# Performance work log

Measured on AMD Instinct MI355X. Metric: run time of the kernel, lower is better.

Reference implementation:

```python
import jax, jax.numpy as jnp
import numpy as np

B, Q, D = 4, 8192, 256
L, P = 2, 8
H0 = W0 = 128
H1 = W1 = 64
EPS = 1e-5


def _bilinear_sample(feat, gx, gy):
    """grid_sample bilinear, padding_mode='border', align_corners=False.
    feat: (B, D, H, W); gx, gy: (B, N) in [-1, 1]. Returns (B, N, D)."""
    b, d, h, w = feat.shape
    # unnormalize (align_corners=False)
    x = ((gx + 1.0) * w - 1.0) * 0.5
    y = ((gy + 1.0) * h - 1.0) * 0.5
    # border padding: clamp coords into valid range
    x = jnp.clip(x, 0.0, w - 1.0)
    y = jnp.clip(y, 0.0, h - 1.0)
    x0 = jnp.floor(x)
    y0 = jnp.floor(y)
    wx = x - x0
    wy = y - y0
    x0i = x0.astype(jnp.int32)
    y0i = y0.astype(jnp.int32)
    x1i = jnp.minimum(x0i + 1, w - 1)
    y1i = jnp.minimum(y0i + 1, h - 1)
    fhw = feat.reshape(b, d, h * w)  # (B, D, H*W)

    def gather(iy, ix):
        idx = iy * w + ix  # (B, N)
        return jnp.take_along_axis(fhw, idx[:, None, :], axis=2)  # (B, D, N)

    v00 = gather(y0i, x0i)
    v01 = gather(y0i, x1i)
    v10 = gather(y1i, x0i)
    v11 = gather(y1i, x1i)
    wxb = wx[:, None, :]
    wyb = wy[:, None, :]
    top = v00 * (1.0 - wxb) + v01 * wxb
    bot = v10 * (1.0 - wxb) + v11 * wxb
    out = top * (1.0 - wyb) + bot * wyb  # (B, D, N)
    return out.transpose(0, 2, 1)  # (B, N, D)


def setup_inputs() -> dict:
    key = jax.random.key(0)
    ks = jax.random.split(key, 12)
    s = 0.02
    return {
        "q": jax.random.normal(ks[0], (B, Q, D), jnp.float32),
        "map0": jax.random.normal(ks[1], (B, D, H0, W0), jnp.float32),
        "map1": jax.random.normal(ks[2], (B, D, H1, W1), jnp.float32),
        "base_ref": jax.random.uniform(ks[3], (B, L, 2), jnp.float32),
        "Wrd": jax.random.normal(ks[4], (D, L * 2), jnp.float32) * s,
        "brd": jax.random.normal(ks[5], (L * 2,), jnp.float32) * s,
        "Woff": jax.random.normal(ks[6], (D, L * P * 2), jnp.float32) * s,
        "boff": jax.random.normal(ks[7], (L * P * 2,), jnp.float32) * 1.5,
        "Wattn": jax.random.normal(ks[8], (D, L * P), jnp.float32) * s,
        "battn": jax.random.normal(ks[9], (L * P,), jnp.float32) * s,
        "Wout": jax.random.normal(ks[10], (D, D), jnp.float32) * s,
        "bout": jax.random.normal(ks[11], (D,), jnp.float32) * s,
    }


def reference(q, map0, map1, base_ref, Wrd, brd, Woff, boff, Wattn, battn, Wout, bout):
    b, qn, d = q.shape
    maps = [map0, map1]
    # per-level reference points, refined through inverse-sigmoid space
    base = jnp.clip(base_ref, EPS, 1.0 - EPS)[:, None, :, :]  # (B, 1, L, 2)
    logit_base = jnp.log(base / (1.0 - base))
    ref_delta = (q @ Wrd + brd).reshape(b, qn, L, 2)
    ref = jax.nn.sigmoid(logit_base + ref_delta)  # (B, Q, L, 2)
    offsets = (q @ Woff + boff).reshape(b, qn, L, P, 2)
    attn_logits = (q @ Wattn + battn).reshape(b, qn, L * P)
    attn = jax.nn.softmax(attn_logits, axis=-1).reshape(b, qn, L, P)

    out = jnp.zeros((b, qn, d), jnp.float32)
    for level, feat in enumerate(maps):
        h, w = feat.shape[2], feat.shape[3]
        normalizer = jnp.array([w, h], jnp.float32)
        loc = ref[:, :, level, None, :] + offsets[:, :, level] / normalizer  # (B,Q,P,2)
        if level == 1:
            loc = jnp.stack([loc[..., 0], jnp.remainder(loc[..., 1], 1.0)], axis=-1)
        loc = loc * 2.0 - 1.0
        gx = loc[..., 0].reshape(b, qn * P)
        gy = loc[..., 1].reshape(b, qn * P)
        samp = _bilinear_sample(feat, gx, gy).reshape(b, qn, P, d)
        out = out + jnp.sum(samp * attn[:, :, level, :, None], axis=2)
    return out @ Wout + bout
```

## Files before the change

### kernel.cpp

```cpp
#include <hip/hip_runtime.h>
#include <hip/hip_bf16.h>

#define BQ 4
#define QN 8192
#define DD 256
#define LL 2
#define H0c 128
#define W0c 128
#define H1c 64
#define W1c 64
#define EPSF 1e-5f

typedef unsigned short ushort_t;
typedef __attribute__((ext_vector_type(8))) short short8;
typedef __attribute__((ext_vector_type(4))) float floatx4;
typedef __attribute__((ext_vector_type(4))) _Float16 half4;

static __device__ __forceinline__ float bf2f(unsigned short u) {
    union { unsigned int u; float f; } x;
    x.u = ((unsigned int)u) << 16;
    return x.f;
}
static __device__ __forceinline__ unsigned short f2bf(float f) {
    __hip_bfloat16 h = __float2bfloat16(f);
    return __builtin_bit_cast(unsigned short, h);
}

__global__ __launch_bounds__(256) void transpose_cast(const float* __restrict__ in,
                                                      __hip_bfloat16* __restrict__ out,
                                                      int HW) {
    __shared__ float tile[32][33];
    int b   = blockIdx.z;
    int hw0 = blockIdx.x * 32;
    int c0  = blockIdx.y * 32;
    const float* inb = in + (size_t)b * DD * HW;
    __hip_bfloat16* outb = out + (size_t)b * DD * HW;
    int tx = threadIdx.x, ty = threadIdx.y;
#pragma unroll
    for (int j = 0; j < 32; j += 8)
        tile[ty + j][tx] = inb[(size_t)(c0 + ty + j) * HW + hw0 + tx];
    __syncthreads();
#pragma unroll
    for (int j = 0; j < 32; j += 8)
        outb[(size_t)(hw0 + ty + j) * DD + c0 + tx] = __float2bfloat16(tile[tx][ty + j]);
}

__global__ __launch_bounds__(256) void pack_wall(const float* __restrict__ Wrd, const float* __restrict__ brd,
                                                 const float* __restrict__ Woff, const float* __restrict__ boff,
                                                 const float* __restrict__ Wattn, const float* __restrict__ battn,
                                                 float* __restrict__ Wall, float* __restrict__ bias64) {
    int idx = blockIdx.x * 256 + threadIdx.x;
    int k = idx >> 6, c = idx & 63;
    float v = (c < 4)  ? Wrd[k * 4 + c]
            : (c < 36) ? Woff[k * 32 + (c - 4)]
            : (c < 52) ? Wattn[k * 16 + (c - 36)]
            : 0.f;
    Wall[idx] = v;
    if (idx < 64) {
        float bv = (idx < 4)  ? brd[idx]
                 : (idx < 36) ? boff[idx - 4]
                 : (idx < 52) ? battn[idx - 36]
                 : 0.f;
        bias64[idx] = bv;
    }
}

__global__ __launch_bounds__(256) void proj_desc(const float* __restrict__ q,
                                                 const float* __restrict__ Wall,
                                                 const float* __restrict__ bias64,
                                                 const float* __restrict__ base_ref,
                                                 int2* __restrict__ dsi,
                                                 half4* __restrict__ dsw) {
    __shared__ float As[32][68];
    __shared__ float Bs[32][64];
    __shared__ float prs[64][68];
    int tid = threadIdx.x;
    int tx = tid & 15, ty = tid >> 4;
    int m0 = blockIdx.x * 64;
    float acc[4][4] = {};

    for (int kt = 0; kt < DD; kt += 32) {
#pragma unroll
        for (int j = 0; j < 8; j++) {
            int e = tid + 256 * j;
            int r = e >> 5, k = e & 31;
            As[k][r] = q[(size_t)(m0 + r) * DD + kt + k];
        }
#pragma unroll
        for (int j = 0; j < 8; j++) {
            int e = tid + 256 * j;
            int k = e >> 6, nn = e & 63;
            Bs[k][nn] = Wall[(size_t)(kt + k) * 64 + nn];
        }
        __syncthreads();
#pragma unroll
        for (int k = 0; k < 32; k++) {
            const float4 a4 = *(const float4*)&As[k][ty * 4];
            const float4 b4 = *(const float4*)&Bs[k][tx * 4];
            acc[0][0] += a4.x * b4.x; acc[0][1] += a4.x * b4.y; acc[0][2] += a4.x * b4.z; acc[0][3] += a4.x * b4.w;
            acc[1][0] += a4.y * b4.x; acc[1][1] += a4.y * b4.y; acc[1][2] += a4.y * b4.z; acc[1][3] += a4.y * b4.w;
            acc[2][0] += a4.z * b4.x; acc[2][1] += a4.z * b4.y; acc[2][2] += a4.z * b4.z; acc[2][3] += a4.z * b4.w;
            acc[3][0] += a4.w * b4.x; acc[3][1] += a4.w * b4.y; acc[3][2] += a4.w * b4.z; acc[3][3] += a4.w * b4.w;
        }
        __syncthreads();
    }

    float4 bias = *(const float4*)&bias64[tx * 4];
#pragma unroll
    for (int i = 0; i < 4; i++) {
        float4 v;
        v.x = acc[i][0] + bias.x;
        v.y = acc[i][1] + bias.y;
        v.z = acc[i][2] + bias.z;
        v.w = acc[i][3] + bias.w;
        *(float4*)&prs[ty * 4 + i][tx * 4] = v;
    }
    __syncthreads();

    int ql = tid >> 2, sq = tid & 3;
    int n = m0 + ql, b = n >> 13;
    const float* p = prs[ql];

    float mx = p[36];
#pragma unroll
    for (int i = 1; i < 16; i++) mx = fmaxf(mx, p[36 + i]);
    float sum = 0.f;
#pragma unroll
    for (int i = 0; i < 16; i++) sum += __expf(p[36 + i] - mx);
    float inv = 1.f / sum;

#pragma unroll
    for (int u = 0; u < 4; u++) {
        int s = sq * 4 + u;
        int l = s >> 3;
        float a = __expf(p[36 + s] - mx) * inv;

        int W = l ? W1c : W0c;
        int H = l ? H1c : H0c;
        float Wf = (float)W, Hf = (float)H;

        float bx = base_ref[(b * LL + l) * 2 + 0];
        float by = base_ref[(b * LL + l) * 2 + 1];
        bx = fminf(fmaxf(bx, EPSF), 1.f - EPSF);
        by = fminf(fmaxf(by, EPSF), 1.f - EPSF);
        float lgx = logf(bx / (1.f - bx));
        float lgy = logf(by / (1.f - by));
        float refx = 1.f / (1.f + __expf(-(lgx + p[l * 2 + 0])));
        float refy = 1.f / (1.f + __expf(-(lgy + p[l * 2 + 1])));

        float locx = refx + p[4 + s * 2 + 0] / Wf;
        float locy = refy + p[4 + s * 2 + 1] / Hf;
        if (l == 1) locy = locy - floorf(locy);

        float gx = locx * 2.f - 1.f;
        float gy = locy * 2.f - 1.f;
        float x = ((gx + 1.f) * Wf - 1.f) * 0.5f;
        float y = ((gy + 1.f) * Hf - 1.f) * 0.5f;
        x = fminf(fmaxf(x, 0.f), Wf - 1.f);
        y = fminf(fmaxf(y, 0.f), Hf - 1.f);
        float x0f = floorf(x), y0f = floorf(y);
        float wx = x - x0f, wy = y - y0f;
        int x0 = (int)x0f, y0 = (int)y0f;
        unsigned int dx = (x0 + 1 <= W - 1) ? DD : 0;
        unsigned int dy = (y0 + 1 <= H - 1) ? (unsigned)(W * DD) : 0;
        int base = ((b * H + y0) * W + x0) * DD;

        float omx = 1.f - wx, omy = 1.f - wy;
        half4 w;
        w[0] = (_Float16)(a * omx * omy);
        w[1] = (_Float16)(a * wx  * omy);
        w[2] = (_Float16)(a * omx * wy);
        w[3] = (_Float16)(a * wx  * wy);

        dsi[(size_t)n * 16 + s] = make_int2(base, (int)((dy << 16) | dx));
        dsw[(size_t)n * 16 + s] = w;
    }
}

__global__ __launch_bounds__(256) void sample_kernel(const ushort_t* __restrict__ mapT0,
                                                     const ushort_t* __restrict__ mapT1,
                                                     const int2* __restrict__ dsi,
                                                     const half4* __restrict__ dsw,
                                                     ushort_t* __restrict__ S) {
    int tid = threadIdx.x;
    int qw = __builtin_amdgcn_readfirstlane(tid >> 6);
    int lx = tid & 63;
    int n = blockIdx.x * 4 + qw;
    int c4 = lx * 4;
    const int2*  gi = dsi + (size_t)n * 16;
    const half4* gw = dsw + (size_t)n * 16;

    float a0 = 0.f, a1 = 0.f, a2 = 0.f, a3 = 0.f;
#pragma unroll
    for (int s = 0; s < 16; s++) {
        int2 g = gi[s];
        half4 wh = gw[s];
        const ushort_t* mp = (s < 8) ? mapT0 : mapT1;
        int dx = g.y & 0xffff;
        int dy = (int)(((unsigned int)g.y) >> 16);
        const ushort_t* p0 = mp + g.x + c4;
        ushort4 u00 = *(const ushort4*)(p0);
        ushort4 u01 = *(const ushort4*)(p0 + dx);
        ushort4 u10 = *(const ushort4*)(p0 + dy);
        ushort4 u11 = *(const ushort4*)(p0 + dx + dy);
        float w00 = (float)wh[0], w01 = (float)wh[1], w10 = (float)wh[2], w11 = (float)wh[3];
        a0 += w00 * bf2f(u00.x) + w01 * bf2f(u01.x) + w10 * bf2f(u10.x) + w11 * bf2f(u11.x);
        a1 += w00 * bf2f(u00.y) + w01 * bf2f(u01.y) + w10 * bf2f(u10.y) + w11 * bf2f(u11.y);
        a2 += w00 * bf2f(u00.z) + w01 * bf2f(u01.z) + w10 * bf2f(u10.z) + w11 * bf2f(u11.z);
        a3 += w00 * bf2f(u00.w) + w01 * bf2f(u01.w) + w10 * bf2f(u10.w) + w11 * bf2f(u11.w);
    }
    ushort4 o;
    o.x = f2bf(a0); o.y = f2bf(a1); o.z = f2bf(a2); o.w = f2bf(a3);
    *(ushort4*)(S + (size_t)n * DD + c4) = o;
}

__global__ __launch_bounds__(256) void out_mfma(const ushort_t* __restrict__ S,
                                                const ushort_t* __restrict__ WT,
                                                const float* __restrict__ bout,
                                                float* __restrict__ out) {
    int wave = threadIdx.x >> 6, lane = threadIdx.x & 63;
    int m0 = blockIdx.x * 64 + wave * 16;
    int mrow = lane & 15, quad = lane >> 4;
    const ushort_t* Sp = S + (size_t)(m0 + mrow) * DD + quad * 8;

    floatx4 acc[16];
#pragma unroll
    for (int nt = 0; nt < 16; nt++) acc[nt] = {0.f, 0.f, 0.f, 0.f};

    for (int k0 = 0; k0 < DD; k0 += 32) {
        short8 a = *(const short8*)(Sp + k0);
#pragma unroll
        for (int nt = 0; nt < 16; nt++) {
            short8 b = *(const short8*)(WT + (size_t)(nt * 16 + mrow) * DD + k0 + quad * 8);
            acc[nt] = __builtin_amdgcn_mfma_f32_16x16x32_bf16(a, b, acc[nt], 0, 0, 0);
        }
    }

    int rbase = quad * 4;
#pragma unroll
    for (int nt = 0; nt < 16; nt++) {
        float bv = bout[nt * 16 + mrow];
#pragma unroll
        for (int r = 0; r < 4; r++) {
            out[(size_t)(m0 + rbase + r) * DD + nt * 16 + mrow] = acc[nt][r] + bv;
        }
    }
}

extern "C" void kernel_launch(void* const* d_in, const int* in_sizes, int n_in,
                              void* d_out, int out_size, void* d_ws, size_t ws_size,
                              hipStream_t stream) {
    const float* q        = (const float*)d_in[0];
    const float* map0     = (const float*)d_in[1];
    const float* map1     = (const float*)d_in[2];
    const float* base_ref = (const float*)d_in[3];
    const float* Wrd      = (const float*)d_in[4];
    const float* brd      = (const float*)d_in[5];
    const float* Woff     = (const float*)d_in[6];
    const float* boff     = (const float*)d_in[7];
    const float* Wattn    = (const float*)d_in[8];
    const float* battn    = (const float*)d_in[9];
    const float* Wout     = (const float*)d_in[10];
    const float* bout     = (const float*)d_in[11];
    float* out = (float*)d_out;

    char* ws = (char*)d_ws;
    __hip_bfloat16* mapT0  = (__hip_bfloat16*)(ws + 0);
    __hip_bfloat16* mapT1  = (__hip_bfloat16*)(ws + 33554432);
    __hip_bfloat16* WoutT  = (__hip_bfloat16*)(ws + 41943040);
    float*          Wall   = (float*)(ws + 42074112);
    float*          bias64 = (float*)(ws + 42139648);
    int2*           dsi    = (int2*)(ws + 42139904);
    half4*          dsw    = (half4*)(ws + 46334208);
    ushort_t*       Sbuf   = (ushort_t*)(ws + 50528512);

    transpose_cast<<<dim3(H0c * W0c / 32, DD / 32, BQ), dim3(32, 8), 0, stream>>>(map0, mapT0, H0c * W0c);
    transpose_cast<<<dim3(H1c * W1c / 32, DD / 32, BQ), dim3(32, 8), 0, stream>>>(map1, mapT1, H1c * W1c);
    transpose_cast<<<dim3(DD / 32, DD / 32, 1), dim3(32, 8), 0, stream>>>(Wout, WoutT, DD);

    pack_wall<<<dim3(64), dim3(256), 0, stream>>>(Wrd, brd, Woff, boff, Wattn, battn, Wall, bias64);

    proj_desc<<<dim3(BQ * QN / 64), dim3(256), 0, stream>>>(q, Wall, bias64, base_ref, dsi, dsw);

    sample_kernel<<<dim3(BQ * QN / 4), dim3(256), 0, stream>>>(
        (const ushort_t*)mapT0, (const ushort_t*)mapT1, dsi, dsw, Sbuf);

    out_mfma<<<dim3(BQ * QN / 64), dim3(256), 0, stream>>>(
        Sbuf, (const ushort_t*)WoutT, bout, out);
}
```

Measured before the change: 289.9 us.

## Fuse prep kernels, widen sampling loads, tile output GEMM with LDS weights

Merges the three transpose-cast launches and the weight packing into one prep kernel, removing launch overhead. The sampler now uses half-waves per query with 16-byte loads of 8 channels, preloads all descriptors, and batches four samples' loads to raise memory-level parallelism; it also sets launch bounds for occupancy. The output GEMM is split across 4 column blocks, with a 64-row Wout slice staged in XOR-swizzled LDS instead of re-read from global memory by every wave. This adds register pressure in the sampler and more blocks in the GEMM.

```diff
diff --git a/kernel.cpp b/kernel.cpp
--- a/kernel.cpp
+++ b/kernel.cpp
@@ -13,29 +13,69 @@
 
 typedef unsigned short ushort_t;
 typedef __attribute__((ext_vector_type(8))) short short8;
+typedef __attribute__((ext_vector_type(8))) unsigned short ushortx8;
 typedef __attribute__((ext_vector_type(4))) float floatx4;
 typedef __attribute__((ext_vector_type(4))) _Float16 half4;
 
-static __device__ __forceinline__ float bf2f(unsigned short u) {
-    union { unsigned int u; float f; } x;
-    x.u = ((unsigned int)u) << 16;
-    return x.f;
+static __device__ __forceinline__ float lo16f(unsigned int d) {
+    union { unsigned int u; float f; } x; x.u = d << 16; return x.f;
+}
+static __device__ __forceinline__ float hi16f(unsigned int d) {
+    union { unsigned int u; float f; } x; x.u = d & 0xFFFF0000u; return x.f;
 }
 static __device__ __forceinline__ unsigned short f2bf(float f) {
     __hip_bfloat16 h = __float2bfloat16(f);
     return __builtin_bit_cast(unsigned short, h);
 }
 
-__global__ __launch_bounds__(256) void transpose_cast(const float* __restrict__ in,
-                                                      __hip_bfloat16* __restrict__ out,
-                                                      int HW) {
+#define T0B 16384
+#define T1B 4096
+#define TWB 64
+__global__ __launch_bounds__(256) void prep(const float* __restrict__ map0, const float* __restrict__ map1,
+                                            const float* __restrict__ Wout,
+                                            const float* __restrict__ Wrd, const float* __restrict__ brd,
+                                            const float* __restrict__ Woff, const float* __restrict__ boff,
+                                            const float* __restrict__ Wattn, const float* __restrict__ battn,
+                                            __hip_bfloat16* __restrict__ mapT0, __hip_bfloat16* __restrict__ mapT1,
+                                            __hip_bfloat16* __restrict__ WoutT,
+                                            float* __restrict__ Wall, float* __restrict__ bias64) {
     __shared__ float tile[32][33];
-    int b   = blockIdx.z;
-    int hw0 = blockIdx.x * 32;
-    int c0  = blockIdx.y * 32;
+    int blk = blockIdx.x;
+    int tx = threadIdx.x, ty = threadIdx.y;
+    const float* in; __hip_bfloat16* outp; int HW, b, c0, hw0;
+    if (blk < T0B) {
+        int l = blk; b = l / (512 * 8); int r = l % (512 * 8);
+        c0 = (r / 512) * 32; hw0 = (r % 512) * 32;
+        in = map0; outp = mapT0; HW = H0c * W0c;
+    } else if (blk < T0B + T1B) {
+        int l = blk - T0B; b = l / (128 * 8); int r = l % (128 * 8);
+        c0 = (r / 128) * 32; hw0 = (r % 128) * 32;
+        in = map1; outp = mapT1; HW = H1c * W1c;
+    } else if (blk < T0B + T1B + TWB) {
+        int l = blk - T0B - T1B; b = 0;
+        c0 = (l / 8) * 32; hw0 = (l % 8) * 32;
+        in = Wout; outp = WoutT; HW = DD;
+    } else {
+        int l = blk - T0B - T1B - TWB;
+        int tid = ty * 32 + tx;
+        int idx = l * 256 + tid;
+        int k = idx >> 6, c = idx & 63;
+        float v = (c < 4)  ? Wrd[k * 4 + c]
+                : (c < 36) ? Woff[k * 32 + (c - 4)]
+                : (c < 52) ? Wattn[k * 16 + (c - 36)]
+                : 0.f;
+        Wall[idx] = v;
+        if (idx < 64) {
+            float bv = (idx < 4)  ? brd[idx]
+                     : (idx < 36) ? boff[idx - 4]
+                     : (idx < 52) ? battn[idx - 36]
+                     : 0.f;
+            bias64[idx] = bv;
+        }
+        return;
+    }
     const float* inb = in + (size_t)b * DD * HW;
-    __hip_bfloat16* outb = out + (size_t)b * DD * HW;
-    int tx = threadIdx.x, ty = threadIdx.y;
+    __hip_bfloat16* outb = outp + (size_t)b * DD * HW;
 #pragma unroll
     for (int j = 0; j < 32; j += 8)
         tile[ty + j][tx] = inb[(size_t)(c0 + ty + j) * HW + hw0 + tx];
@@ -43,26 +83,6 @@
 #pragma unroll
     for (int j = 0; j < 32; j += 8)
         outb[(size_t)(hw0 + ty + j) * DD + c0 + tx] = __float2bfloat16(tile[tx][ty + j]);
-}
-
-__global__ __launch_bounds__(256) void pack_wall(const float* __restrict__ Wrd, const float* __restrict__ brd,
-                                                 const float* __restrict__ Woff, const float* __restrict__ boff,
-                                                 const float* __restrict__ Wattn, const float* __restrict__ battn,
-                                                 float* __restrict__ Wall, float* __restrict__ bias64) {
-    int idx = blockIdx.x * 256 + threadIdx.x;
-    int k = idx >> 6, c = idx & 63;
-    float v = (c < 4)  ? Wrd[k * 4 + c]
-            : (c < 36) ? Woff[k * 32 + (c - 4)]
-            : (c < 52) ? Wattn[k * 16 + (c - 36)]
-            : 0.f;
-    Wall[idx] = v;
-    if (idx < 64) {
-        float bv = (idx < 4)  ? brd[idx]
-                 : (idx < 36) ? boff[idx - 4]
-                 : (idx < 52) ? battn[idx - 36]
-                 : 0.f;
-        bias64[idx] = bv;
-    }
 }
 
 __global__ __launch_bounds__(256) void proj_desc(const float* __restrict__ q,
@@ -177,72 +197,109 @@
     }
 }
 
-__global__ __launch_bounds__(256) void sample_kernel(const ushort_t* __restrict__ mapT0,
-                                                     const ushort_t* __restrict__ mapT1,
-                                                     const int2* __restrict__ dsi,
-                                                     const half4* __restrict__ dsw,
-                                                     ushort_t* __restrict__ S) {
+__global__ __launch_bounds__(256, 3) void sample_kernel(const ushort_t* __restrict__ mapT0,
+                                                        const ushort_t* __restrict__ mapT1,
+                                                        const int2* __restrict__ dsi,
+                                                        const half4* __restrict__ dsw,
+                                                        ushort_t* __restrict__ S) {
     int tid = threadIdx.x;
-    int qw = __builtin_amdgcn_readfirstlane(tid >> 6);
     int lx = tid & 63;
-    int n = blockIdx.x * 4 + qw;
-    int c4 = lx * 4;
+    int n = blockIdx.x * 8 + (tid >> 6) * 2 + (lx >> 5);
+    int c8 = (lx & 31) * 8;
     const int2*  gi = dsi + (size_t)n * 16;
     const half4* gw = dsw + (size_t)n * 16;
 
-    float a0 = 0.f, a1 = 0.f, a2 = 0.f, a3 = 0.f;
-#pragma unroll
-    for (int s = 0; s < 16; s++) {
-        int2 g = gi[s];
-        half4 wh = gw[s];
-        const ushort_t* mp = (s < 8) ? mapT0 : mapT1;
-        int dx = g.y & 0xffff;
-        int dy = (int)(((unsigned int)g.y) >> 16);
-        const ushort_t* p0 = mp + g.x + c4;
-        ushort4 u00 = *(const ushort4*)(p0);
-        ushort4 u01 = *(const ushort4*)(p0 + dx);
-        ushort4 u10 = *(const ushort4*)(p0 + dy);
-        ushort4 u11 = *(const ushort4*)(p0 + dx + dy);
-        float w00 = (float)wh[0], w01 = (float)wh[1], w10 = (float)wh[2], w11 = (float)wh[3];
-        a0 += w00 * bf2f(u00.x) + w01 * bf2f(u01.x) + w10 * bf2f(u10.x) + w11 * bf2f(u11.x);
-        a1 += w00 * bf2f(u00.y) + w01 * bf2f(u01.y) + w10 * bf2f(u10.y) + w11 * bf2f(u11.y);
-        a2 += w00 * bf2f(u00.z) + w01 * bf2f(u01.z) + w10 * bf2f(u10.z) + w11 * bf2f(u11.z);
-        a3 += w00 * bf2f(u00.w) + w01 * bf2f(u01.w) + w10 * bf2f(u10.w) + w11 * bf2f(u11.w);
-    }
-    ushort4 o;
-    o.x = f2bf(a0); o.y = f2bf(a1); o.z = f2bf(a2); o.w = f2bf(a3);
-    *(ushort4*)(S + (size_t)n * DD + c4) = o;
+    int2 g[16]; half4 wh[16];
+#pragma unroll
+    for (int s = 0; s < 16; s++) { g[s] = gi[s]; wh[s] = gw[s]; }
+
+    float acc[8];
+#pragma unroll
+    for (int i = 0; i < 8; i++) acc[i] = 0.f;
+
+#pragma unroll
+    for (int grp = 0; grp < 4; grp++) {
+        const ushort_t* mp = (grp < 2) ? mapT0 : mapT1;
+        uint4 u[4][4];
+#pragma unroll
+        for (int j = 0; j < 4; j++) {
+            int s = grp * 4 + j;
+            int dx = g[s].y & 0xffff;
+            int dy = (int)(((unsigned int)g[s].y) >> 16);
+            const ushort_t* p0 = mp + g[s].x + c8;
+            u[j][0] = *(const uint4*)(p0);
+            u[j][1] = *(const uint4*)(p0 + dx);
+            u[j][2] = *(const uint4*)(p0 + dy);
+            u[j][3] = *(const uint4*)(p0 + dx + dy);
+        }
+#pragma unroll
+        for (int j = 0; j < 4; j++) {
+            int s = grp * 4 + j;
+            float w0 = (float)wh[s][0], w1 = (float)wh[s][1], w2 = (float)wh[s][2], w3 = (float)wh[s][3];
+#pragma unroll
+            for (int corner = 0; corner < 4; corner++) {
+                uint4 v = u[j][corner];
+                float wc = (corner == 0) ? w0 : (corner == 1) ? w1 : (corner == 2) ? w2 : w3;
+                acc[0] += wc * lo16f(v.x); acc[1] += wc * hi16f(v.x);
+                acc[2] += wc * lo16f(v.y); acc[3] += wc * hi16f(v.y);
+                acc[4] += wc * lo16f(v.z); acc[5] += wc * hi16f(v.z);
+                acc[6] += wc * lo16f(v.w); acc[7] += wc * hi16f(v.w);
+            }
+        }
+    }
+    ushortx8 o;
+#pragma unroll
+    for (int i = 0; i < 8; i++) o[i] = f2bf(acc[i]);
+    *(ushortx8*)(S + (size_t)n * DD + c8) = o;
 }
 
 __global__ __launch_bounds__(256) void out_mfma(const ushort_t* __restrict__ S,
                                                 const ushort_t* __restrict__ WT,
                                                 const float* __restrict__ bout,
                                                 float* __restrict__ out) {
-    int wave = threadIdx.x >> 6, lane = threadIdx.x & 63;
-    int m0 = blockIdx.x * 64 + wave * 16;
+    __shared__ ushort_t wlds[64][256];
+    int tid = threadIdx.x;
+    int n0c = blockIdx.x * 64;
+    int wave = tid >> 6, lane = tid & 63;
+    int m0 = blockIdx.y * 64 + wave * 16;
     int mrow = lane & 15, quad = lane >> 4;
+
+#pragma unroll
+    for (int i = 0; i < 8; i++) {
+        int idx = tid + 256 * i;
+        int row = idx >> 5, c = idx & 31;
+        *(uint4*)&wlds[row][(c ^ (row & 31)) * 8] =
+            *(const uint4*)(WT + (size_t)(n0c + row) * DD + c * 8);
+    }
+    __syncthreads();
+
     const ushort_t* Sp = S + (size_t)(m0 + mrow) * DD + quad * 8;
-
-    floatx4 acc[16];
-#pragma unroll
-    for (int nt = 0; nt < 16; nt++) acc[nt] = {0.f, 0.f, 0.f, 0.f};
-
-    for (int k0 = 0; k0 < DD; k0 += 32) {
-        short8 a = *(const short8*)(Sp + k0);
-#pragma unroll
-        for (int nt = 0; nt < 16; nt++) {
-            short8 b = *(const short8*)(WT + (size_t)(nt * 16 + mrow) * DD + k0 + quad * 8);
-            acc[nt] = __builtin_amdgcn_mfma_f32_16x16x32_bf16(a, b, acc[nt], 0, 0, 0);
+    short8 a[8];
+#pragma unroll
+    for (int k = 0; k < 8; k++) a[k] = *(const short8*)(Sp + k * 32);
+
+    floatx4 acc[4];
+#pragma unroll
+    for (int nt = 0; nt < 4; nt++) acc[nt] = {0.f, 0.f, 0.f, 0.f};
+
+#pragma unroll
+    for (int nt = 0; nt < 4; nt++) {
+        int row = nt * 16 + mrow;
+#pragma unroll
+        for (int k = 0; k < 8; k++) {
+            int c = k * 4 + quad;
+            short8 b = *(const short8*)&wlds[row][(c ^ (row & 31)) * 8];
+            acc[nt] = __builtin_amdgcn_mfma_f32_16x16x32_bf16(a[k], b, acc[nt], 0, 0, 0);
         }
     }
 
     int rbase = quad * 4;
 #pragma unroll
-    for (int nt = 0; nt < 16; nt++) {
-        float bv = bout[nt * 16 + mrow];
+    for (int nt = 0; nt < 4; nt++) {
+        float bv = bout[n0c + nt * 16 + mrow];
 #pragma unroll
         for (int r = 0; r < 4; r++) {
-            out[(size_t)(m0 + rbase + r) * DD + nt * 16 + mrow] = acc[nt][r] + bv;
+            out[(size_t)(m0 + rbase + r) * DD + n0c + nt * 16 + mrow] = acc[nt][r] + bv;
         }
     }
 }
@@ -274,17 +331,15 @@
     half4*          dsw    = (half4*)(ws + 46334208);
     ushort_t*       Sbuf   = (ushort_t*)(ws + 50528512);
 
-    transpose_cast<<<dim3(H0c * W0c / 32, DD / 32, BQ), dim3(32, 8), 0, stream>>>(map0, mapT0, H0c * W0c);
-    transpose_cast<<<dim3(H1c * W1c / 32, DD / 32, BQ), dim3(32, 8), 0, stream>>>(map1, mapT1, H1c * W1c);
-    transpose_cast<<<dim3(DD / 32, DD / 32, 1), dim3(32, 8), 0, stream>>>(Wout, WoutT, DD);
-
-    pack_wall<<<dim3(64), dim3(256), 0, stream>>>(Wrd, brd, Woff, boff, Wattn, battn, Wall, bias64);
+    prep<<<dim3(T0B + T1B + TWB + 64), dim3(32, 8), 0, stream>>>(
+        map0, map1, Wout, Wrd, brd, Woff, boff, Wattn, battn,
+        mapT0, mapT1, WoutT, Wall, bias64);
 
     proj_desc<<<dim3(BQ * QN / 64), dim3(256), 0, stream>>>(q, Wall, bias64, base_ref, dsi, dsw);
 
-    sample_kernel<<<dim3(BQ * QN / 4), dim3(256), 0, stream>>>(
+    sample_kernel<<<dim3(BQ * QN / 8), dim3(256), 0, stream>>>(
         (const ushort_t*)mapT0, (const ushort_t*)mapT1, dsi, dsw, Sbuf);
 
-    out_mfma<<<dim3(BQ * QN / 64), dim3(256), 0, stream>>>(
+    out_mfma<<<dim3(4, BQ * QN / 64), dim3(256), 0, stream>>>(
         Sbuf, (const ushort_t*)WoutT, bout, out);
 }
```

After: 246.3 us. -15.0%, faster.
